# Performance work log

Measured on AMD Instinct MI355X. Metric: run time of the kernel, lower is better.

## Reference

```python
import jax, jax.numpy as jnp
import numpy as np

N = 131072        # number of input vectors
DIM = 256         # e_dim
NUM_VQ = 4        # residual stages
K = 512           # codebook_size
BETA = 0.2
N_EMOTIONS = 7


def setup_inputs() -> dict:
    key = jax.random.key(0)
    k1, k2, k3 = jax.random.split(key, 3)
    return {
        "input_vector": jax.random.normal(k1, (N, DIM), dtype=jnp.float32),
        # stacked codebooks for the num_vq VectorQuantize layers
        "codebooks": jax.random.normal(k2, (NUM_VQ, K, DIM), dtype=jnp.float32),
        # frozen random code -> emotion map (buffer, int)
        "code_to_emotion_map": jax.random.randint(k3, (K,), 0, N_EMOTIONS, dtype=jnp.int32),
    }


def _vq(x, cb):
    """Nearest-codebook lookup with straight-through estimator.
    x: [N, D], cb: [K, D] -> (quantized [N, D], indices [N])."""
    d = (jnp.sum(x * x, axis=1, keepdims=True)
         - 2.0 * (x @ cb.T)
         + jnp.sum(cb * cb, axis=1))
    idx = jnp.argmin(d, axis=1)
    q = cb[idx]                                  # gather [N, D]
    q_st = x + jax.lax.stop_gradient(q - x)      # straight-through
    return q_st, idx


def reference(input_vector, codebooks, code_to_emotion_map):
    residual = input_vector
    total_vq_loss = jnp.zeros((), dtype=input_vector.dtype)
    quantized_codes = []
    perplexities = []
    first_indices = None
    inv_n = 1.0 / input_vector.shape[0]
    for i in range(NUM_VQ):
        quantized, indices = _vq(residual, codebooks[i])
        vq_loss = (jnp.mean((jax.lax.stop_gradient(residual) - quantized) ** 2)
                   + BETA * jnp.mean((residual - jax.lax.stop_gradient(quantized)) ** 2))
        total_vq_loss = total_vq_loss + vq_loss
        # perplexity from one-hot histogram (no grad); scatter-add instead of dense one-hot
        e_mean = jnp.zeros((K,), dtype=jnp.float32).at[indices].add(inv_n)
        perplexities.append(jnp.exp(-jnp.sum(e_mean * jnp.log(e_mean + 1e-10))))
        residual = residual - jax.lax.stop_gradient(quantized)
        quantized_codes.append(quantized)
        if i == 0:
            first_indices = indices
    final_quantized = jnp.concatenate(quantized_codes, axis=1)  # [N, NUM_VQ*DIM]
    logits = code_to_emotion_map[first_indices]                 # [N] int
    return final_quantized, total_vq_loss, logits, jnp.stack(perplexities)
```

## Files before the change

### kernel.cpp

```cpp
#include <hip/hip_runtime.h>

#define N_VEC 131072
#define DIM 256
#define KCODES 512
#define NUM_VQ 4

constexpr float BETA = 0.2f;
constexpr int BM = 64;
constexpr int NTHREADS = 512;
constexpr int NBLOCKS = N_VEC / BM;
constexpr float WMARGIN = 1.0f;
constexpr int MAXCAND = 24;

typedef short bf16x8 __attribute__((ext_vector_type(8)));
typedef float f32x4  __attribute__((ext_vector_type(4)));

__device__ __forceinline__ unsigned short f2bf(float x) {
    unsigned u = __builtin_bit_cast(unsigned, x);
    u += 0x7FFF + ((u >> 16) & 1);
    return (unsigned short)(u >> 16);
}
__device__ __forceinline__ float bf2f(unsigned short h) {
    unsigned u = ((unsigned)h) << 16;
    return __builtin_bit_cast(float, u);
}

__global__ void norms_kernel(const float* __restrict__ cb, float* __restrict__ norms,
                             int* __restrict__ hist) {
    if (blockIdx.x < 8) hist[blockIdx.x * 256 + threadIdx.x] = 0;
    int row = blockIdx.x * 4 + (threadIdx.x >> 6);
    int lane = threadIdx.x & 63;
    const float* r = cb + (size_t)row * DIM;
    float4 v = *(const float4*)(r + lane * 4);
    float s = v.x * v.x + v.y * v.y + v.z * v.z + v.w * v.w;
    #pragma unroll
    for (int off = 32; off; off >>= 1) s += __shfl_down(s, off);
    if (lane == 0) norms[row] = s;
}

__global__ void bprep_kernel(const float* __restrict__ cb, char* __restrict__ bp) {
    int id = blockIdx.x * 256 + threadIdx.x;
    int lane = id & 63;
    int ct   = (id >> 6) & 31;
    int ks   = (id >> 11) & 7;
    int s    = id >> 14;
    int col  = ct * 16 + (lane & 15);
    int kb   = ks * 32 + (lane >> 4) * 8;
    const float* src = cb + ((size_t)(s * KCODES + col)) * DIM + kb;
    float4 v0 = *(const float4*)src;
    float4 v1 = *(const float4*)(src + 4);
    float xs[8] = {v0.x, v0.y, v0.z, v0.w, v1.x, v1.y, v1.z, v1.w};
    bf16x8 o;
    #pragma unroll
    for (int i = 0; i < 8; ++i) o[i] = (short)f2bf(xs[i]);
    size_t off = (((size_t)(s * 8 + ks)) * 32 + ct) * 1024 + (size_t)lane * 16;
    *(bf16x8*)(bp + off) = o;
}

__global__ __launch_bounds__(NTHREADS, 4)
void vq_fused(const float* __restrict__ x,
              const char* __restrict__ bp,
              const float* __restrict__ cb,
              const float* __restrict__ norms,
              float* __restrict__ out,
              float* __restrict__ sq_partials,
              int* __restrict__ hist,
              const int* __restrict__ emap,
              float* __restrict__ logits)
{
    __shared__ __align__(16) char Ahi[32768];
    __shared__ __align__(16) char Alo[32768];
    __shared__ float ns[KCODES];
    __shared__ float wmin[8][BM];
    __shared__ float smin[BM];
    __shared__ int   cnt[BM];
    __shared__ int   cand[BM][MAXCAND];
    __shared__ int   sidx[BM];

    const int tid  = threadIdx.x;
    const int w    = tid >> 6;
    const int lane = tid & 63;
    const int l15  = lane & 15;
    const int h16  = lane >> 4;
    const long row0 = (long)blockIdx.x * BM;

    #pragma unroll
    for (int e = 0; e < 4; ++e) {
        int ga = e * 512 + tid;
        int row = ga >> 5, k8 = ga & 31;
        const float* src = x + (row0 + row) * (long)DIM + k8 * 8;
        float4 v0 = *(const float4*)src;
        float4 v1 = *(const float4*)(src + 4);
        float xs[8] = {v0.x, v0.y, v0.z, v0.w, v1.x, v1.y, v1.z, v1.w};
        bf16x8 h, l;
        #pragma unroll
        for (int i = 0; i < 8; ++i) {
            unsigned short hb = f2bf(xs[i]);
            h[i] = (short)hb;
            l[i] = (short)f2bf(xs[i] - bf2f(hb));
        }
        int off = (row << 9) + ((k8 ^ (row & 7)) << 4);
        *(bf16x8*)(Ahi + off) = h;
        *(bf16x8*)(Alo + off) = l;
    }

    float lsq_acc = 0.f;

    #pragma unroll 1
    for (int s = 0; s < NUM_VQ; ++s) {
        ns[tid] = norms[s * KCODES + tid];
        __syncthreads();

        f32x4 acc[4][4];
        #pragma unroll
        for (int t = 0; t < 4; ++t)
            #pragma unroll
            for (int c = 0; c < 4; ++c)
                acc[t][c] = (f32x4){0.f, 0.f, 0.f, 0.f};

        const char* bw = bp + (size_t)s * 262144 + (size_t)(w * 4) * 1024 + (size_t)lane * 16;

        #pragma unroll
        for (int ks = 0; ks < 8; ++ks) {
            bf16x8 ah[4];
            #pragma unroll
            for (int t = 0; t < 4; ++t) {
                int row = t * 16 + l15;
                int k8  = ks * 4 + h16;
                int off = (row << 9) + ((k8 ^ (row & 7)) << 4);
                ah[t] = *(const bf16x8*)(Ahi + off);
            }
            #pragma unroll
            for (int c = 0; c < 4; ++c) {
                bf16x8 bh = *(const bf16x8*)(bw + (size_t)ks * 32768 + (size_t)c * 1024);
                __builtin_amdgcn_s_setprio(1);
                #pragma unroll
                for (int t = 0; t < 4; ++t)
                    acc[t][c] = __builtin_amdgcn_mfma_f32_16x16x32_bf16(ah[t], bh, acc[t][c], 0, 0, 0);
                __builtin_amdgcn_s_setprio(0);
            }
        }

        #pragma unroll
        for (int t = 0; t < 4; ++t) {
            #pragma unroll
            for (int r = 0; r < 4; ++r) {
                float bv = 3.4e38f;
                #pragma unroll
                for (int c = 0; c < 4; ++c) {
                    int col = w * 64 + c * 16 + l15;
                    float sc = ns[col] - 2.0f * acc[t][c][r];
                    bv = fminf(bv, sc);
                }
                #pragma unroll
                for (int m = 1; m < 16; m <<= 1)
                    bv = fminf(bv, __shfl_xor(bv, m));
                if (l15 == 0) wmin[w][t * 16 + h16 * 4 + r] = bv;
            }
        }
        __syncthreads();
        if (tid < BM) {
            float bv = wmin[0][tid];
            #pragma unroll
            for (int q2 = 1; q2 < 8; ++q2) bv = fminf(bv, wmin[q2][tid]);
            smin[tid] = bv;
            cnt[tid] = 0;
        }
        __syncthreads();

        #pragma unroll
        for (int t = 0; t < 4; ++t) {
            #pragma unroll
            for (int r = 0; r < 4; ++r) {
                int row = t * 16 + h16 * 4 + r;
                float thr = smin[row] + WMARGIN;
                #pragma unroll
                for (int c = 0; c < 4; ++c) {
                    int col = w * 64 + c * 16 + l15;
                    float sc = ns[col] - 2.0f * acc[t][c][r];
                    if (sc <= thr) {
                        int pos = atomicAdd(&cnt[row], 1);
                        if (pos < MAXCAND) cand[row][pos] = col;
                    }
                }
            }
        }
        __syncthreads();

        const float* cbs_s = cb + (size_t)s * KCODES * DIM;
        #pragma unroll 1
        for (int i = 0; i < 8; ++i) {
            int row = w * 8 + i;
            int n = cnt[row]; if (n > MAXCAND) n = MAXCAND;
            if (n == 1) {
                if (lane == 0) sidx[row] = cand[row][0];
                continue;
            }
            float bs = 3.4e38f; int bcol = KCODES;
            int g  = lane >> 4;
            int lg = lane & 15;
            for (int j0 = 0; j0 < n; j0 += 4) {
                int j = j0 + g;
                int col = cand[row][(j < n) ? j : 0];
                float part = 0.f;
                #pragma unroll
                for (int gg = 0; gg < 2; ++gg) {
                    int k8 = 2 * lg + gg;
                    int off = (row << 9) + ((k8 ^ (row & 7)) << 4);
                    bf16x8 h = *(const bf16x8*)(Ahi + off);
                    bf16x8 l = *(const bf16x8*)(Alo + off);
                    const float* cp = cbs_s + (size_t)col * DIM + k8 * 8;
                    float4 c0 = *(const float4*)cp;
                    float4 c1 = *(const float4*)(cp + 4);
                    float cs[8] = {c0.x, c0.y, c0.z, c0.w, c1.x, c1.y, c1.z, c1.w};
                    #pragma unroll
                    for (int d = 0; d < 8; ++d) {
                        float xv = bf2f((unsigned short)h[d]) + bf2f((unsigned short)l[d]);
                        part += xv * cs[d];
                    }
                }
                #pragma unroll
                for (int m = 1; m < 16; m <<= 1) part += __shfl_xor(part, m);
                float sc = ns[col] - 2.0f * part;
                #pragma unroll
                for (int m = 16; m < 64; m <<= 1) {
                    float ov = __shfl_xor(sc, m);
                    int   ok = __shfl_xor(col, m);
                    if (ov < sc || (ov == sc && ok < col)) { sc = ov; col = ok; }
                }
                if (sc < bs || (sc == bs && col < bcol)) { bs = sc; bcol = col; }
            }
            if (lane == 0) sidx[row] = bcol;
        }
        __syncthreads();

        const int lrow = tid >> 3;
        const int kidx = sidx[lrow];
        const long grow = row0 + lrow;
        const float* cbr = cb + ((size_t)s * KCODES + kidx) * DIM;
        float* qr = out + grow * 1024 + s * DIM;
        #pragma unroll
        for (int e = 0; e < 4; ++e) {
            int k8 = (tid & 7) + 8 * e;
            int off = (lrow << 9) + ((k8 ^ (lrow & 7)) << 4);
            bf16x8 h = *(const bf16x8*)(Ahi + off);
            bf16x8 l = *(const bf16x8*)(Alo + off);
            float4 c0 = *(const float4*)(cbr + k8 * 8);
            float4 c1 = *(const float4*)(cbr + k8 * 8 + 4);
            float cs[8] = {c0.x, c0.y, c0.z, c0.w, c1.x, c1.y, c1.z, c1.w};
            float qv[8], rv[8];
            #pragma unroll
            for (int i = 0; i < 8; ++i) {
                float xv = bf2f((unsigned short)h[i]) + bf2f((unsigned short)l[i]);
                qv[i] = xv + (cs[i] - xv);
                rv[i] = xv - qv[i];
                lsq_acc += rv[i] * rv[i];
            }
            *(float4*)(qr + k8 * 8)     = (float4){qv[0], qv[1], qv[2], qv[3]};
            *(float4*)(qr + k8 * 8 + 4) = (float4){qv[4], qv[5], qv[6], qv[7]};
            if (s < NUM_VQ - 1) {
                bf16x8 nh, nl;
                #pragma unroll
                for (int i = 0; i < 8; ++i) {
                    unsigned short hb = f2bf(rv[i]);
                    nh[i] = (short)hb;
                    nl[i] = (short)f2bf(rv[i] - bf2f(hb));
                }
                *(bf16x8*)(Ahi + off) = nh;
                *(bf16x8*)(Alo + off) = nl;
            }
        }

        if (tid < BM) atomicAdd(&hist[s * KCODES + sidx[tid]], 1);
        if (s == 0 && tid < BM) logits[row0 + tid] = (float)emap[sidx[tid]];
    }

    #pragma unroll
    for (int off = 32; off; off >>= 1) lsq_acc += __shfl_down(lsq_acc, off);
    if (lane == 0) sq_partials[blockIdx.x * 8 + w] = lsq_acc;
}

__global__ void finalize_kernel(const float* __restrict__ sq_partials,
                                const int* __restrict__ hist,
                                float* __restrict__ loss_out,
                                float* __restrict__ perp_out)
{
    __shared__ float sred[8];
    int tid = threadIdx.x;
    float s = 0.f;
    for (int i = tid; i < NBLOCKS * 8; i += 512) s += sq_partials[i];
    #pragma unroll
    for (int off = 32; off; off >>= 1) s += __shfl_down(s, off);
    if ((tid & 63) == 0) sred[tid >> 6] = s;
    __syncthreads();
    if (tid == 0) {
        float t = 0.f;
        for (int i = 0; i < 8; ++i) t += sred[i];
        *loss_out = (1.f + BETA) * t / ((float)N_VEC * (float)DIM);
    }
    for (int st = 0; st < NUM_VQ; ++st) {
        __syncthreads();
        float e = (float)hist[st * 512 + tid] * (1.f / (float)N_VEC);
        float term = e * logf(e + 1e-10f);
        #pragma unroll
        for (int off = 32; off; off >>= 1) term += __shfl_down(term, off);
        if ((tid & 63) == 0) sred[tid >> 6] = term;
        __syncthreads();
        if (tid == 0) {
            float t = 0.f;
            for (int i = 0; i < 8; ++i) t += sred[i];
            perp_out[st] = expf(-t);
        }
    }
}

extern "C" void kernel_launch(void* const* d_in, const int* in_sizes, int n_in,
                              void* d_out, int out_size, void* d_ws, size_t ws_size,
                              hipStream_t stream) {
    const float* x    = (const float*)d_in[0];
    const float* cbs  = (const float*)d_in[1];
    const int*   emap = (const int*)d_in[2];
    float* out = (float*)d_out;

    const size_t QSZ = (size_t)N_VEC * (NUM_VQ * DIM);
    float* loss_out = out + QSZ;
    float* logits   = out + QSZ + 1;
    float* perp     = out + QSZ + 1 + N_VEC;

    float* sq_partials = (float*)d_ws;
    int*   hist        = (int*)(sq_partials + NBLOCKS * 8);
    float* norms       = (float*)(hist + NUM_VQ * KCODES);
    char*  bprep       = (char*)(norms + NUM_VQ * KCODES);

    norms_kernel<<<NUM_VQ * KCODES / 4, 256, 0, stream>>>(cbs, norms, hist);
    bprep_kernel<<<256, 256, 0, stream>>>(cbs, bprep);

    vq_fused<<<NBLOCKS, NTHREADS, 0, stream>>>(
        x, bprep, cbs, norms, out, sq_partials, hist, emap, logits);

    finalize_kernel<<<1, 512, 0, stream>>>(sq_partials, hist, loss_out, perp);
}
```

Before: 520.6 us.

## Precompute scores in registers, hoist codebook loads, simplify straight-through output

```diff
diff --git a/kernel.cpp b/kernel.cpp
--- a/kernel.cpp
+++ b/kernel.cpp
@@ -141,17 +141,23 @@
             }
         }
 
+        float nsc[4];
+        #pragma unroll
+        for (int c = 0; c < 4; ++c) nsc[c] = ns[w * 64 + c * 16 + l15];
+        #pragma unroll
+        for (int t = 0; t < 4; ++t)
+            #pragma unroll
+            for (int c = 0; c < 4; ++c)
+                #pragma unroll
+                for (int r = 0; r < 4; ++r)
+                    acc[t][c][r] = nsc[c] - 2.0f * acc[t][c][r];
+
         #pragma unroll
         for (int t = 0; t < 4; ++t) {
             #pragma unroll
             for (int r = 0; r < 4; ++r) {
-                float bv = 3.4e38f;
-                #pragma unroll
-                for (int c = 0; c < 4; ++c) {
-                    int col = w * 64 + c * 16 + l15;
-                    float sc = ns[col] - 2.0f * acc[t][c][r];
-                    bv = fminf(bv, sc);
-                }
+                float bv = fminf(fminf(acc[t][0][r], acc[t][1][r]),
+                                 fminf(acc[t][2][r], acc[t][3][r]));
                 #pragma unroll
                 for (int m = 1; m < 16; m <<= 1)
                     bv = fminf(bv, __shfl_xor(bv, m));
@@ -176,11 +182,9 @@
                 float thr = smin[row] + WMARGIN;
                 #pragma unroll
                 for (int c = 0; c < 4; ++c) {
-                    int col = w * 64 + c * 16 + l15;
-                    float sc = ns[col] - 2.0f * acc[t][c][r];
-                    if (sc <= thr) {
+                    if (acc[t][c][r] <= thr) {
                         int pos = atomicAdd(&cnt[row], 1);
-                        if (pos < MAXCAND) cand[row][pos] = col;
+                        if (pos < MAXCAND) cand[row][pos] = w * 64 + c * 16 + l15;
                     }
                 }
             }
@@ -205,7 +209,7 @@
                 float part = 0.f;
                 #pragma unroll
                 for (int gg = 0; gg < 2; ++gg) {
-                    int k8 = 2 * lg + gg;
+                    int k8 = lg + 16 * gg;
                     int off = (row << 9) + ((k8 ^ (row & 7)) << 4);
                     bf16x8 h = *(const bf16x8*)(Ahi + off);
                     bf16x8 l = *(const bf16x8*)(Alo + off);
@@ -239,25 +243,30 @@
         const long grow = row0 + lrow;
         const float* cbr = cb + ((size_t)s * KCODES + kidx) * DIM;
         float* qr = out + grow * 1024 + s * DIM;
+        float4 cc[8];
+        #pragma unroll
+        for (int e = 0; e < 4; ++e) {
+            int k8 = (tid & 7) + 8 * e;
+            cc[2 * e]     = *(const float4*)(cbr + k8 * 8);
+            cc[2 * e + 1] = *(const float4*)(cbr + k8 * 8 + 4);
+        }
         #pragma unroll
         for (int e = 0; e < 4; ++e) {
             int k8 = (tid & 7) + 8 * e;
             int off = (lrow << 9) + ((k8 ^ (lrow & 7)) << 4);
             bf16x8 h = *(const bf16x8*)(Ahi + off);
             bf16x8 l = *(const bf16x8*)(Alo + off);
-            float4 c0 = *(const float4*)(cbr + k8 * 8);
-            float4 c1 = *(const float4*)(cbr + k8 * 8 + 4);
-            float cs[8] = {c0.x, c0.y, c0.z, c0.w, c1.x, c1.y, c1.z, c1.w};
-            float qv[8], rv[8];
+            float cs[8] = {cc[2*e].x, cc[2*e].y, cc[2*e].z, cc[2*e].w,
+                           cc[2*e+1].x, cc[2*e+1].y, cc[2*e+1].z, cc[2*e+1].w};
+            float rv[8];
             #pragma unroll
             for (int i = 0; i < 8; ++i) {
                 float xv = bf2f((unsigned short)h[i]) + bf2f((unsigned short)l[i]);
-                qv[i] = xv + (cs[i] - xv);
-                rv[i] = xv - qv[i];
+                rv[i] = xv - cs[i];
                 lsq_acc += rv[i] * rv[i];
             }
-            *(float4*)(qr + k8 * 8)     = (float4){qv[0], qv[1], qv[2], qv[3]};
-            *(float4*)(qr + k8 * 8 + 4) = (float4){qv[4], qv[5], qv[6], qv[7]};
+            *(float4*)(qr + k8 * 8)     = cc[2 * e];
+            *(float4*)(qr + k8 * 8 + 4) = cc[2 * e + 1];
             if (s < NUM_VQ - 1) {
                 bf16x8 nh, nl;
                 #pragma unroll
```

Result: slower. 559.2 us (+7.4%).
